# Kernel tuning notes

Measured on AMD Instinct MI355X. Metric: run time of the kernel, lower is better.

Reference implementation:

```python
import jax, jax.numpy as jnp
import numpy as np

# B groups, N packed tokens/group, D model dim, H heads, L layers, FF mlp hidden,
# M samples packed per group, C classes, PD patch_dim, NF/NT freq/time pos tables
B, N, D, H, L, FF, M, C, PD, NF, NT = 4, 1024, 768, 12, 12, 3072, 8, 527, 256, 8, 64


def _ln(x, g, b, eps=1e-6):
    m = jnp.mean(x, -1, keepdims=True)
    v = jnp.mean((x - m) ** 2, -1, keepdims=True)
    return (x - m) * jax.lax.rsqrt(v + eps) * g + b


def _attn(xq, xkv, Wq, bq, Wkv, bkv, Wo, bo, allowed):
    # allowed: [b, i, j] bool; faithful to source: NO 1/sqrt(d_head) scaling.
    b, i, _ = xq.shape
    j = xkv.shape[1]
    q = (xq @ Wq + bq).reshape(b, i, H, -1).transpose(0, 2, 1, 3)
    k, v = jnp.split(xkv @ Wkv + bkv, 2, axis=-1)
    k = k.reshape(b, j, H, -1).transpose(0, 2, 1, 3)
    v = v.reshape(b, j, H, -1).transpose(0, 2, 1, 3)
    dots = jnp.einsum('bhid,bhjd->bhij', q, k)
    neg = -jnp.finfo(dots.dtype).max
    dots = jnp.where(allowed[:, None, :, :], dots, neg)
    a = jax.nn.softmax(dots, axis=-1)
    out = jnp.einsum('bhij,bhjd->bhid', a, v).transpose(0, 2, 1, 3).reshape(b, i, -1)
    return out @ Wo + bo


def setup_inputs() -> dict:
    ks = iter(jax.random.split(jax.random.key(0), 48))
    rn = lambda shape, s=0.02: jax.random.normal(next(ks), shape, jnp.float32) * s
    return {
        'patches': jax.random.normal(next(ks), (B, N, PD), jnp.float32),
        'sample_ids': jnp.sort(jax.random.randint(next(ks), (B, N), 0, M), axis=-1).astype(jnp.int32),
        'key_pad': jnp.ones((B, N), bool),
        'freq_idx': jax.random.randint(next(ks), (B, N), 0, NF).astype(jnp.int32),
        'time_idx': jax.random.randint(next(ks), (B, N), 0, NT).astype(jnp.int32),
        'patch_W': rn((PD, D)), 'patch_b': jnp.zeros((D,)),
        'pos_f': rn((NF, D), 1.0), 'pos_t': rn((NT, D), 1.0),
        'ln1_g': jnp.ones((L, D)), 'ln1_b': jnp.zeros((L, D)),
        'Wq': rn((L, D, D)), 'bq': jnp.zeros((L, D)),
        'Wkv': rn((L, D, 2 * D)), 'bkv': jnp.zeros((L, 2 * D)),
        'Wo': rn((L, D, D)), 'bo': jnp.zeros((L, D)),
        'ln2_g': jnp.ones((L, D)), 'ln2_b': jnp.zeros((L, D)),
        'W1': rn((L, D, FF)), 'b1': jnp.zeros((L, FF)),
        'W2': rn((L, FF, D)), 'b2': jnp.zeros((L, D)),
        'norm_g': jnp.ones((D,)), 'norm_b': jnp.zeros((D,)),
        'pool_q': rn((D,), 1.0),
        'pool_Wq': rn((D, D)), 'pool_bq': jnp.zeros((D,)),
        'pool_Wkv': rn((D, 2 * D)), 'pool_bkv': jnp.zeros((2 * D,)),
        'pool_Wo': rn((D, D)), 'pool_bo': jnp.zeros((D,)),
        'mln_g': jnp.ones((D,)), 'mln_b': jnp.zeros((D,)),
        'head_W': rn((D, C)), 'head_b': jnp.zeros((C,)),
    }


def reference(patches, sample_ids, key_pad, freq_idx, time_idx, patch_W, patch_b, pos_f, pos_t,
              ln1_g, ln1_b, Wq, bq, Wkv, bkv, Wo, bo, ln2_g, ln2_b, W1, b1, W2, b2,
              norm_g, norm_b, pool_q, pool_Wq, pool_bq, pool_Wkv, pool_bkv, pool_Wo, pool_bo,
              mln_g, mln_b, head_W, head_b):
    # patch embed + factorized freq/time positional embedding
    x = patches @ patch_W + patch_b + pos_f[freq_idx] + pos_t[time_idx]  # [B, N, D]
    # block-diagonal attention within each packed sample + key-padding mask
    same = sample_ids[:, :, None] == sample_ids[:, None, :]
    allowed = same & key_pad[:, None, :]
    for l in range(L):
        h = _ln(x, ln1_g[l], ln1_b[l])
        x = x + _attn(h, h, Wq[l], bq[l], Wkv[l], bkv[l], Wo[l], bo[l], allowed)
        h = _ln(x, ln2_g[l], ln2_b[l])
        x = x + (jax.nn.gelu(h @ W1[l] + b1[l], approximate=False) @ W2[l] + b2[l])
    x = _ln(x, norm_g, norm_b)
    # attention pooling: one learned query per packed sample, attends only its own tokens
    queries = jnp.broadcast_to(pool_q, (B, M, D))
    pool_allowed = (sample_ids[:, None, :] == jnp.arange(M)[None, :, None]) & key_pad[:, None, :]
    pooled = _attn(queries, x, pool_Wq, pool_bq, pool_Wkv, pool_bkv, pool_Wo, pool_bo, pool_allowed)
    return _ln(pooled, mln_g, mln_b) @ head_W + head_b  # [B, M, C]
```

## Files before the change

### kernel.cpp

```cpp
#include <hip/hip_runtime.h>
#include <hip/hip_bf16.h>
#include <math.h>

#define BB   4
#define NN   1024
#define DD   768
#define HHH  12
#define LLL  12
#define FFD  3072
#define MMM  8
#define CCC  527
#define PDIM 256

typedef unsigned short u16;
typedef __attribute__((ext_vector_type(8))) short bf16x8;
typedef __attribute__((ext_vector_type(4))) float f32x4;

__device__ inline float b2f(u16 x) {
    union { float f; unsigned u; } c; c.u = ((unsigned)x) << 16; return c.f;
}
__device__ inline u16 f2b(float f) {
    __hip_bfloat16 h = __float2bfloat16(f);
    return *reinterpret_cast<u16*>(&h);
}

__device__ __forceinline__ void gl_lds16(const u16* g, const u16* l) {
    __builtin_amdgcn_global_load_lds(
        (const __attribute__((address_space(1))) unsigned int*)(unsigned long long)g,
        (__attribute__((address_space(3))) unsigned int*)(unsigned)(unsigned long long)l,
        16, 0, 0);
}

__global__ void k_pad_norm(const void* __restrict__ p, unsigned char* __restrict__ out, int n) {
    __shared__ int isInt;
    const int t = threadIdx.x;
    if (t == 0) isInt = 1;
    __syncthreads();
    const unsigned* up = (const unsigned*)p;
    for (int i = t; i < n / 4; i += 1024) {
        unsigned v = up[i];
        if (v > 1u) isInt = 0;
    }
    __syncthreads();
    const int* ip = (const int*)p;
    const unsigned char* cp = (const unsigned char*)p;
    const int mode = isInt;
    for (int i = t; i < n; i += 1024)
        out[i] = mode ? (unsigned char)(ip[i] != 0) : (unsigned char)(cp[i] != 0);
}

__global__ __launch_bounds__(256) void k_transpose_cvt(
    const float* __restrict__ src, u16* __restrict__ dst,
    int K, int N, long srcLS, long dstLS)
{
    __shared__ float t[32][33];
    const float* s = src + (size_t)blockIdx.z * srcLS;
    u16* d = dst + (size_t)blockIdx.z * dstLS;
    int n0 = blockIdx.x * 32, k0 = blockIdx.y * 32;
    int tx = threadIdx.x & 31, ty = threadIdx.x >> 5;
    #pragma unroll
    for (int i = 0; i < 32; i += 8)
        t[ty + i][tx] = s[(size_t)(k0 + ty + i) * N + n0 + tx];
    __syncthreads();
    #pragma unroll
    for (int i = 0; i < 32; i += 8)
        d[(size_t)(n0 + ty + i) * K + k0 + tx] = f2b(t[tx][ty + i]);
}

__global__ __launch_bounds__(256) void k_cvt(const float* __restrict__ s, u16* __restrict__ d, int n4) {
    int i = blockIdx.x * 256 + threadIdx.x;
    if (i >= n4) return;
    float4 v = ((const float4*)s)[i];
    union { u16 h[4]; uint2 u; } o;
    o.h[0] = f2b(v.x); o.h[1] = f2b(v.y); o.h[2] = f2b(v.z); o.h[3] = f2b(v.w);
    ((uint2*)d)[i] = o.u;
}

__global__ __launch_bounds__(256) void k_bias_pack(const float* __restrict__ bq,
                                                   const float* __restrict__ bkv,
                                                   float* __restrict__ bqkv) {
    int i = blockIdx.x * 256 + threadIdx.x;
    if (i >= LLL * 2304) return;
    int l = i / 2304, c = i % 2304;
    bqkv[i] = (c < 768) ? bq[l * 768 + c] : bkv[l * 1536 + (c - 768)];
}

__global__ void k_ranges(const int* __restrict__ sid, int2* __restrict__ qr, int2* __restrict__ pr) {
    int b = blockIdx.x, t = threadIdx.x;
    const int* s = sid + b * NN;
    if (t < 16) {
        int lo_id = s[t * 64], hi_id = s[t * 64 + 63];
        int lo = 0, hi = NN;
        while (lo < hi) { int mid = (lo + hi) >> 1; if (s[mid] < lo_id) lo = mid + 1; else hi = mid; }
        int l2 = 0, h2 = NN;
        while (l2 < h2) { int mid = (l2 + h2) >> 1; if (s[mid] <= hi_id) l2 = mid + 1; else h2 = mid; }
        qr[b * 16 + t] = make_int2(lo, l2);
    }
    if (t < MMM) {
        int l2 = 0, h2 = NN;
        while (l2 < h2) { int mid = (l2 + h2) >> 1; if (s[mid] < t) l2 = mid + 1; else h2 = mid; }
        int l3 = 0, h3 = NN;
        while (l3 < h3) { int mid = (l3 + h3) >> 1; if (s[mid] <= t) l3 = mid + 1; else h3 = mid; }
        pr[b * MMM + t] = make_int2(l2, l3);
    }
}

__device__ inline void stv(u16* p, float v) { *p = f2b(v); }
__device__ inline void stv(float* p, float v) { *p = v; }

template <typename OT>
__global__ __launch_bounds__(256) void k_ln(const float* __restrict__ x,
                                            const float* __restrict__ g,
                                            const float* __restrict__ b,
                                            OT* __restrict__ out) {
    int row = blockIdx.x;
    const float* xr = x + (size_t)row * DD;
    int t = threadIdx.x;
    float v[3], s1 = 0.f, s2 = 0.f;
    #pragma unroll
    for (int i = 0; i < 3; i++) { v[i] = xr[t + i * 256]; s1 += v[i]; s2 += v[i] * v[i]; }
    #pragma unroll
    for (int o = 32; o; o >>= 1) { s1 += __shfl_xor(s1, o); s2 += __shfl_xor(s2, o); }
    __shared__ float a1[4], a2[4];
    int w = t >> 6;
    if ((t & 63) == 0) { a1[w] = s1; a2[w] = s2; }
    __syncthreads();
    s1 = a1[0] + a1[1] + a1[2] + a1[3];
    s2 = a2[0] + a2[1] + a2[2] + a2[3];
    float mean = s1 * (1.f / DD);
    float var = s2 * (1.f / DD) - mean * mean;
    float rstd = rsqrtf(fmaxf(var, 0.f) + 1e-6f);
    #pragma unroll
    for (int i = 0; i < 3; i++) {
        int c = t + i * 256;
        stv(&out[(size_t)row * DD + c], (v[i] - mean) * rstd * g[c] + b[c]);
    }
}

template <int EPI, int BM>
__global__ __launch_bounds__(256) void k_gemm(
    const u16* __restrict__ A, int lda,
    const u16* __restrict__ Bt, int ldb,
    const float* __restrict__ bias,
    float* __restrict__ Cf, u16* __restrict__ Cb,
    const float* __restrict__ resid,
    int ldc, int K)
{
    constexpr int NR  = (BM == 128) ? 4 : 2;
    constexpr int ASZ = BM * 32;
    constexpr int BSZ = 128 * 32;
    __shared__ __align__(16) u16 As[3][ASZ];
    __shared__ __align__(16) u16 Bs[3][BSZ];
    const int row0 = blockIdx.y * BM, col0 = blockIdx.x * 128;
    const int t = threadIdx.x;
    const int w = t >> 6, lane = t & 63;
    const int wr = (BM == 128) ? (w >> 1) * 64 : 0;
    const int wc = (BM == 128) ? (w & 1) * 64 : w * 32;
    const int fr = lane & 15, fg = lane >> 4;
    const int srow = t >> 2, sseg = (t & 3) * 8;
    const u16* Ap = A + (size_t)(row0 + srow) * lda + sseg;
    const u16* Bp = Bt + (size_t)(col0 + srow) * ldb + sseg;
    const size_t lstep = (size_t)64 * lda, bstep = (size_t)64 * ldb;

    auto stage = [&](int buf, int k0) {
        #pragma unroll
        for (int i = 0; i < BM / 64; i++)
            gl_lds16(Ap + i * lstep + k0, &As[buf][i * 2048 + t * 8]);
        #pragma unroll
        for (int i = 0; i < 2; i++)
            gl_lds16(Bp + i * bstep + k0, &Bs[buf][i * 2048 + t * 8]);
    };

    f32x4 acc[4][NR];
    #pragma unroll
    for (int m = 0; m < 4; m++)
        #pragma unroll
        for (int n = 0; n < NR; n++) acc[m][n] = (f32x4){0.f, 0.f, 0.f, 0.f};

    const int nt = K >> 5;
    stage(0, 0);
    stage(1, 32);

    for (int kt = 0; kt < nt; ++kt) {
        if (kt + 1 < nt) {
            if constexpr (BM == 128) asm volatile("s_waitcnt vmcnt(4)" ::: "memory");
            else                     asm volatile("s_waitcnt vmcnt(3)" ::: "memory");
        } else {
            asm volatile("s_waitcnt vmcnt(0)" ::: "memory");
        }
        __builtin_amdgcn_s_barrier();
        __builtin_amdgcn_sched_barrier(0);
        if (kt + 2 < nt) stage((kt + 2) % 3, (kt + 2) * 32);
        const int cur = kt % 3;
        bf16x8 af[4], bfr[NR];
        #pragma unroll
        for (int m = 0; m < 4; m++) af[m] = *(const bf16x8*)&As[cur][(wr + m * 16 + fr) * 32 + fg * 8];
        #pragma unroll
        for (int n = 0; n < NR; n++) bfr[n] = *(const bf16x8*)&Bs[cur][(wc + n * 16 + fr) * 32 + fg * 8];
        #pragma unroll
        for (int m = 0; m < 4; m++)
            #pragma unroll
            for (int n = 0; n < NR; n++)
                acc[m][n] = __builtin_amdgcn_mfma_f32_16x16x32_bf16(af[m], bfr[n], acc[m][n], 0, 0, 0);
    }
    #pragma unroll
    for (int m = 0; m < 4; m++) {
        #pragma unroll
        for (int n = 0; n < NR; n++) {
            const int col = col0 + wc + n * 16 + fr;
            const float bb = bias[col];
            #pragma unroll
            for (int r = 0; r < 4; r++) {
                const size_t row = row0 + wr + m * 16 + fg * 4 + r;
                float v = acc[m][n][r] + bb;
                if (EPI == 0) {
                    Cb[row * ldc + col] = f2b(v);
                } else if (EPI == 1) {
                    Cf[row * ldc + col] = v + resid[row * ldc + col];
                } else if (EPI == 2) {
                    float gl = 0.5f * v * (1.f + erff(v * 0.70710678118f));
                    Cb[row * ldc + col] = f2b(gl);
                } else {
                    Cf[row * ldc + col] = v;
                }
            }
        }
    }
}

__global__ __launch_bounds__(256) void k_attn(
    const u16* __restrict__ qkv,
    const int* __restrict__ sid, const unsigned char* __restrict__ pad,
    const int2* __restrict__ qr,
    u16* __restrict__ outb)
{
    __shared__ __align__(16) u16 Qs[64][72];
    __shared__ __align__(16) u16 Ks[64][72];
    __shared__ __align__(16) u16 Vt[64][72];
    __shared__ __align__(16) u16 Ps[4][16][72];
    __shared__ int sidq[64];
    __shared__ int sidj[64];
    __shared__ int padj[64];
    const int b = blockIdx.z, h = blockIdx.y, qt = blockIdx.x;
    const int i0 = qt * 64;
    const int t = threadIdx.x, w = t >> 6, lane = t & 63;
    const int fr = lane & 15, fg = lane >> 4;
    const int srow = t >> 2, sseg = (t & 3) * 16;
    const size_t tokbase = (size_t)b * NN;
    const u16* qbase = qkv + (tokbase + i0) * 2304 + h * 64;
    *(uint4*)&Qs[srow][sseg]     = *(const uint4*)(qbase + (size_t)srow * 2304 + sseg);
    *(uint4*)&Qs[srow][sseg + 8] = *(const uint4*)(qbase + (size_t)srow * 2304 + sseg + 8);
    if (t < 64) sidq[t] = sid[tokbase + i0 + t];
    __syncthreads();
    bf16x8 qf0 = *(const bf16x8*)&Qs[w * 16 + fr][fg * 8];
    bf16x8 qf1 = *(const bf16x8*)&Qs[w * 16 + fr][32 + fg * 8];
    const int myrow = w * 16 + fg * 4;
    float m_run[4], l_run[4];
    f32x4 oacc[4];
    #pragma unroll
    for (int r = 0; r < 4; r++) { m_run[r] = -1e30f; l_run[r] = 0.f; }
    #pragma unroll
    for (int n = 0; n < 4; n++) oacc[n] = (f32x4){0.f, 0.f, 0.f, 0.f};
    const int2 rg = qr[b * 16 + qt];
    const u16* kbase = qkv + tokbase * 2304 + 768 + h * 64;
    const u16* vbase = qkv + tokbase * 2304 + 1536 + h * 64;

    for (int j0 = rg.x & ~63; j0 < rg.y; j0 += 64) {
        __syncthreads();
        *(uint4*)&Ks[srow][sseg]     = *(const uint4*)(kbase + (size_t)(j0 + srow) * 2304 + sseg);
        *(uint4*)&Ks[srow][sseg + 8] = *(const uint4*)(kbase + (size_t)(j0 + srow) * 2304 + sseg + 8);
        {
            uint4 v0 = *(const uint4*)(vbase + (size_t)(j0 + srow) * 2304 + sseg);
            uint4 v1 = *(const uint4*)(vbase + (size_t)(j0 + srow) * 2304 + sseg + 8);
            u16 tmp[16];
            *(uint4*)&tmp[0] = v0;
            *(uint4*)&tmp[8] = v1;
            #pragma unroll
            for (int e = 0; e < 16; e++) Vt[sseg + e][srow] = tmp[e];
        }
        if (t < 64) {
            sidj[t] = sid[tokbase + j0 + t];
            padj[t] = pad[tokbase + j0 + t];
        }
        __syncthreads();
        f32x4 s[4];
        #pragma unroll
        for (int nj = 0; nj < 4; nj++) {
            bf16x8 kf0 = *(const bf16x8*)&Ks[nj * 16 + fr][fg * 8];
            bf16x8 kf1 = *(const bf16x8*)&Ks[nj * 16 + fr][32 + fg * 8];
            f32x4 a = (f32x4){0.f, 0.f, 0.f, 0.f};
            a = __builtin_amdgcn_mfma_f32_16x16x32_bf16(qf0, kf0, a, 0, 0, 0);
            a = __builtin_amdgcn_mfma_f32_16x16x32_bf16(qf1, kf1, a, 0, 0, 0);
            s[nj] = a;
        }
        #pragma unroll
        for (int nj = 0; nj < 4; nj++) {
            const int jj = nj * 16 + fr;
            const int sj = sidj[jj];
            const int pd = padj[jj];
            #pragma unroll
            for (int r = 0; r < 4; r++) {
                const bool ok = pd && (sj == sidq[myrow + r]);
                s[nj][r] = ok ? s[nj][r] : -3e38f;
            }
        }
        float mnew[4], scale[4];
        #pragma unroll
        for (int r = 0; r < 4; r++) {
            float mx = fmaxf(fmaxf(s[0][r], s[1][r]), fmaxf(s[2][r], s[3][r]));
            #pragma unroll
            for (int o = 1; o < 16; o <<= 1) mx = fmaxf(mx, __shfl_xor(mx, o));
            mnew[r] = fmaxf(m_run[r], mx);
            scale[r] = __expf(m_run[r] - mnew[r]);
            m_run[r] = mnew[r];
        }
        #pragma unroll
        for (int r = 0; r < 4; r++) {
            float rs = 0.f;
            #pragma unroll
            for (int nj = 0; nj < 4; nj++) {
                float pv = __expf(s[nj][r] - mnew[r]);
                rs += pv;
                Ps[w][fg * 4 + r][nj * 16 + fr] = f2b(pv);
            }
            #pragma unroll
            for (int o = 1; o < 16; o <<= 1) rs += __shfl_xor(rs, o);
            l_run[r] = l_run[r] * scale[r] + rs;
        }
        #pragma unroll
        for (int n = 0; n < 4; n++)
            #pragma unroll
            for (int r = 0; r < 4; r++) oacc[n][r] *= scale[r];
        bf16x8 pa0 = *(const bf16x8*)&Ps[w][fr][fg * 8];
        bf16x8 pa1 = *(const bf16x8*)&Ps[w][fr][32 + fg * 8];
        #pragma unroll
        for (int nd = 0; nd < 4; nd++) {
            bf16x8 vf0 = *(const bf16x8*)&Vt[nd * 16 + fr][fg * 8];
            bf16x8 vf1 = *(const bf16x8*)&Vt[nd * 16 + fr][32 + fg * 8];
            oacc[nd] = __builtin_amdgcn_mfma_f32_16x16x32_bf16(pa0, vf0, oacc[nd], 0, 0, 0);
            oacc[nd] = __builtin_amdgcn_mfma_f32_16x16x32_bf16(pa1, vf1, oacc[nd], 0, 0, 0);
        }
    }
    float inv[4];
    #pragma unroll
    for (int r = 0; r < 4; r++) inv[r] = 1.f / l_run[r];
    #pragma unroll
    for (int nd = 0; nd < 4; nd++)
        #pragma unroll
        for (int r = 0; r < 4; r++)
            outb[(tokbase + i0 + myrow + r) * DD + h * 64 + nd * 16 + fr] = f2b(oacc[nd][r] * inv[r]);
}

__global__ __launch_bounds__(256) void k_posadd(float* __restrict__ x,
                                                const int* __restrict__ fidx, const int* __restrict__ tidx,
                                                const float* __restrict__ pf, const float* __restrict__ pt) {
    int row = blockIdx.x;
    int fi = fidx[row], ti = tidx[row];
    for (int c = threadIdx.x; c < DD; c += 256)
        x[(size_t)row * DD + c] += pf[(size_t)fi * DD + c] + pt[(size_t)ti * DD + c];
}

__global__ __launch_bounds__(64) void k_qvec(const float* __restrict__ pq, const float* __restrict__ Wq,
                                             const float* __restrict__ bq, float* __restrict__ qv) {
    int c = blockIdx.x;
    int l = threadIdx.x;
    float s = 0.f;
    #pragma unroll
    for (int d = l; d < DD; d += 64) s += pq[d] * Wq[(size_t)d * DD + c];
    #pragma unroll
    for (int o = 32; o; o >>= 1) s += __shfl_xor(s, o);
    if (l == 0) qv[c] = s + bq[c];
}

__global__ __launch_bounds__(256) void k_pool_attn(
    const float* __restrict__ qv, const u16* __restrict__ kv,
    const unsigned char* __restrict__ pad, const int2* __restrict__ pr,
    float* __restrict__ outp)
{
    const int idx = blockIdx.x;
    const int h = idx % HHH, bm = idx / HHH;
    const int b = bm >> 3, m = bm & 7;
    const int2 rg = pr[b * MMM + m];
    const int lo = rg.x, cnt = rg.y - rg.x;
    __shared__ float sc[NN];
    __shared__ float qsh[64];
    __shared__ float rbuf[4];
    __shared__ float vacc[4][64];
    if (threadIdx.x < 64) qsh[threadIdx.x] = qv[h * 64 + threadIdx.x];
    __syncthreads();
    for (int j = threadIdx.x; j < cnt; j += 256) {
        const u16* krow = kv + (size_t)(b * NN + lo + j) * 1536 + h * 64;
        float s = 0.f;
        #pragma unroll
        for (int dv = 0; dv < 8; dv++) {
            bf16x8 k8 = *(const bf16x8*)(krow + dv * 8);
            #pragma unroll
            for (int e = 0; e < 8; e++) s += qsh[dv * 8 + e] * b2f((u16)k8[e]);
        }
        sc[j] = pad[b * NN + lo + j] ? s : -3e38f;
    }
    __syncthreads();
    float mx = -3e38f;
    for (int j = threadIdx.x; j < cnt; j += 256) mx = fmaxf(mx, sc[j]);
    #pragma unroll
    for (int o = 32; o; o >>= 1) mx = fmaxf(mx, __shfl_xor(mx, o));
    if ((threadIdx.x & 63) == 0) rbuf[threadIdx.x >> 6] = mx;
    __syncthreads();
    mx = fmaxf(fmaxf(rbuf[0], rbuf[1]), fmaxf(rbuf[2], rbuf[3]));
    __syncthreads();
    float sm = 0.f;
    for (int j = threadIdx.x; j < cnt; j += 256) { float p = __expf(sc[j] - mx); sc[j] = p; sm += p; }
    #pragma unroll
    for (int o = 32; o; o >>= 1) sm += __shfl_xor(sm, o);
    if ((threadIdx.x & 63) == 0) rbuf[threadIdx.x >> 6] = sm;
    __syncthreads();
    sm = rbuf[0] + rbuf[1] + rbuf[2] + rbuf[3];
    const float inv = 1.f / sm;
    {
        const int d = threadIdx.x & 63, g = threadIdx.x >> 6;
        float acc = 0.f;
        for (int j = g; j < cnt; j += 4)
            acc += sc[j] * b2f(kv[(size_t)(b * NN + lo + j) * 1536 + 768 + h * 64 + d]);
        vacc[g][d] = acc;
        __syncthreads();
        if (g == 0)
            outp[(size_t)(b * MMM + m) * DD + h * 64 + d] =
                (vacc[0][d] + vacc[1][d] + vacc[2][d] + vacc[3][d]) * inv;
    }
}

__global__ __launch_bounds__(256) void k_small_mm(const float* __restrict__ A, const float* __restrict__ W,
                                                  const float* __restrict__ bias, float* __restrict__ out,
                                                  int N, int Kd) {
    const int row = blockIdx.y;
    const int cl = threadIdx.x & 63, kg = threadIdx.x >> 6;
    const int c = blockIdx.x * 64 + cl;
    const int cload = (c < N) ? c : (N - 1);
    __shared__ float As[DD];
    __shared__ float red[4][64];
    for (int d = threadIdx.x; d < Kd; d += 256) As[d] = A[(size_t)row * Kd + d];
    __syncthreads();
    const int kper = Kd >> 2;
    const int kbase = kg * kper;
    float s = 0.f;
    const float* w = W + (size_t)kbase * N + cload;
    #pragma unroll 4
    for (int i = 0; i < kper; i++) s += As[kbase + i] * w[(size_t)i * N];
    red[kg][cl] = s;
    __syncthreads();
    if (kg == 0 && c < N)
        out[(size_t)row * N + c] = red[0][cl] + red[1][cl] + red[2][cl] + red[3][cl] + bias[c];
}

extern "C" void kernel_launch(void* const* d_in, const int* in_sizes, int n_in,
                              void* d_out, int out_size, void* d_ws, size_t ws_size,
                              hipStream_t stream) {
    const float* patches   = (const float*)d_in[0];
    const int*   sample_ids= (const int*)d_in[1];
    const void*  key_pad_raw = (const void*)d_in[2];
    const int*   freq_idx  = (const int*)d_in[3];
    const int*   time_idx  = (const int*)d_in[4];
    const float* patch_W   = (const float*)d_in[5];
    const float* patch_b   = (const float*)d_in[6];
    const float* pos_f     = (const float*)d_in[7];
    const float* pos_t     = (const float*)d_in[8];
    const float* ln1_g     = (const float*)d_in[9];
    const float* ln1_b     = (const float*)d_in[10];
    const float* Wq        = (const float*)d_in[11];
    const float* bq        = (const float*)d_in[12];
    const float* Wkv       = (const float*)d_in[13];
    const float* bkv       = (const float*)d_in[14];
    const float* Wo        = (const float*)d_in[15];
    const float* bo        = (const float*)d_in[16];
    const float* ln2_g     = (const float*)d_in[17];
    const float* ln2_b     = (const float*)d_in[18];
    const float* W1        = (const float*)d_in[19];
    const float* b1        = (const float*)d_in[20];
    const float* W2        = (const float*)d_in[21];
    const float* b2        = (const float*)d_in[22];
    const float* norm_g    = (const float*)d_in[23];
    const float* norm_b    = (const float*)d_in[24];
    const float* pool_q    = (const float*)d_in[25];
    const float* pool_Wq   = (const float*)d_in[26];
    const float* pool_bq   = (const float*)d_in[27];
    const float* pool_Wkv  = (const float*)d_in[28];
    const float* pool_bkv  = (const float*)d_in[29];
    const float* pool_Wo   = (const float*)d_in[30];
    const float* pool_bo   = (const float*)d_in[31];
    const float* mln_g     = (const float*)d_in[32];
    const float* mln_b     = (const float*)d_in[33];
    const float* head_W    = (const float*)d_in[34];
    const float* head_b    = (const float*)d_in[35];
    float* outp = (float*)d_out;
    (void)in_sizes; (void)n_in; (void)out_size; (void)ws_size;

    char* ws = (char*)d_ws;
    size_t off = 0;
    auto alloc = [&](size_t bytes) -> void* {
        void* p = (void*)(ws + off);
        off += (bytes + 255) & ~(size_t)255;
        return p;
    };
    u16* WqkvT    = (u16*)alloc((size_t)LLL * 2304 * 768 * 2);
    u16* WoT      = (u16*)alloc((size_t)LLL * 768 * 768 * 2);
    u16* W1T      = (u16*)alloc((size_t)LLL * 3072 * 768 * 2);
    u16* W2T      = (u16*)alloc((size_t)LLL * 768 * 3072 * 2);
    u16* patchWT  = (u16*)alloc((size_t)768 * 256 * 2);
    u16* poolWkvT = (u16*)alloc((size_t)1536 * 768 * 2);
    float* bqkv   = (float*)alloc((size_t)LLL * 2304 * 4);
    unsigned char* pad_u8 = (unsigned char*)alloc(BB * NN);
    float* x      = (float*)alloc((size_t)4096 * 768 * 4);
    u16* hbuf     = (u16*)alloc((size_t)4096 * 768 * 2);
    u16* qkvb     = (u16*)alloc((size_t)4096 * 2304 * 2);
    u16* attno    = (u16*)alloc((size_t)4096 * 768 * 2);
    u16* mid      = (u16*)alloc((size_t)4096 * 3072 * 2);
    u16* patch_bf = mid;
    u16* xn       = attno;
    u16* poolkv   = qkvb;
    float* qvec   = (float*)alloc(768 * 4);
    float* pooled_pre = (float*)alloc(32 * 768 * 4);
    float* pooled2    = (float*)alloc(32 * 768 * 4);
    float* mlnout     = (float*)alloc(32 * 768 * 4);
    int2* qr = (int2*)alloc(4 * 16 * sizeof(int2));
    int2* pr = (int2*)alloc(4 * 8 * sizeof(int2));

    k_pad_norm<<<1, 1024, 0, stream>>>(key_pad_raw, pad_u8, BB * NN);
    k_transpose_cvt<<<dim3(24, 24, LLL), 256, 0, stream>>>(Wq, WqkvT, 768, 768, (long)768 * 768, (long)2304 * 768);
    k_transpose_cvt<<<dim3(48, 24, LLL), 256, 0, stream>>>(Wkv, WqkvT + (size_t)768 * 768, 768, 1536, (long)768 * 1536, (long)2304 * 768);
    k_transpose_cvt<<<dim3(24, 24, LLL), 256, 0, stream>>>(Wo, WoT, 768, 768, (long)768 * 768, (long)768 * 768);
    k_transpose_cvt<<<dim3(96, 24, LLL), 256, 0, stream>>>(W1, W1T, 768, 3072, (long)768 * 3072, (long)3072 * 768);
    k_transpose_cvt<<<dim3(24, 96, LLL), 256, 0, stream>>>(W2, W2T, 3072, 768, (long)3072 * 768, (long)768 * 3072);
    k_transpose_cvt<<<dim3(24, 8, 1), 256, 0, stream>>>(patch_W, patchWT, 256, 768, 0, 0);
    k_transpose_cvt<<<dim3(48, 24, 1), 256, 0, stream>>>(pool_Wkv, poolWkvT, 768, 1536, 0, 0);
    k_cvt<<<1024, 256, 0, stream>>>(patches, patch_bf, 4096 * 256 / 4);
    k_bias_pack<<<(LLL * 2304 + 255) / 256, 256, 0, stream>>>(bq, bkv, bqkv);
    k_ranges<<<4, 64, 0, stream>>>(sample_ids, qr, pr);

    k_gemm<3, 64><<<dim3(6, 64), 256, 0, stream>>>(patch_bf, 256, patchWT, 256, patch_b, x, nullptr, nullptr, 768, 256);
    k_posadd<<<4096, 256, 0, stream>>>(x, freq_idx, time_idx, pos_f, pos_t);

    for (int l = 0; l < LLL; l++) {
        k_ln<u16><<<4096, 256, 0, stream>>>(x, ln1_g + l * 768, ln1_b + l * 768, hbuf);
        k_gemm<0, 128><<<dim3(18, 32), 256, 0, stream>>>(hbuf, 768, WqkvT + (size_t)l * 2304 * 768, 768,
                                                         bqkv + l * 2304, nullptr, qkvb, nullptr, 2304, 768);
        k_attn<<<dim3(16, 12, 4), 256, 0, stream>>>(qkvb, sample_ids, pad_u8, qr, attno);
        k_gemm<1, 64><<<dim3(6, 64), 256, 0, stream>>>(attno, 768, WoT + (size_t)l * 768 * 768, 768,
                                                       bo + l * 768, x, nullptr, x, 768, 768);
        k_ln<u16><<<4096, 256, 0, stream>>>(x, ln2_g + l * 768, ln2_b + l * 768, hbuf);
        k_gemm<2, 128><<<dim3(24, 32), 256, 0, stream>>>(hbuf, 768, W1T + (size_t)l * 3072 * 768, 768,
                                                         b1 + l * 3072, nullptr, mid, nullptr, 3072, 768);
        k_gemm<1, 64><<<dim3(6, 64), 256, 0, stream>>>(mid, 3072, W2T + (size_t)l * 768 * 3072, 3072,
                                                       b2 + l * 768, x, nullptr, x, 768, 3072);
    }

    k_ln<u16><<<4096, 256, 0, stream>>>(x, norm_g, norm_b, xn);
    k_gemm<0, 128><<<dim3(12, 32), 256, 0, stream>>>(xn, 768, poolWkvT, 768, pool_bkv, nullptr, poolkv, nullptr, 1536, 768);
    k_qvec<<<768, 64, 0, stream>>>(pool_q, pool_Wq, pool_bq, qvec);
    k_pool_attn<<<BB * MMM * HHH, 256, 0, stream>>>(qvec, poolkv, pad_u8, pr, pooled_pre);
    k_small_mm<<<dim3(12, 32), 256, 0, stream>>>(pooled_pre, pool_Wo, pool_bo, pooled2, 768, 768);
    k_ln<float><<<32, 256, 0, stream>>>(pooled2, mln_g, mln_b, mlnout);
    k_small_mm<<<dim3(9, 32), 256, 0, stream>>>(mlnout, head_W, head_b, outp, 527, 768);
}
```

Measured before the change: 2.178 ms.

## Swizzle GEMM blocks across XCDs, prefetch attention K/V, skew V layout

The GEMM kernel remaps its linear block id so that, when the grid size is a multiple of 8, each XCD gets a contiguous range of output tiles. The aim is better L2 reuse of the A and B panels. The attention kernel now loads the next K/V tile, sample ids and pad flags into registers while the current tile is being computed, overlapping global loads with MFMA work. The transposed V buffer in LDS gets a per-16-row skew to cut bank conflicts on the scattered transpose writes. The costs are extra registers for the prefetch and some more index arithmetic.

```diff
diff --git a/kernel.cpp b/kernel.cpp
--- a/kernel.cpp
+++ b/kernel.cpp
@@ -151,7 +151,11 @@
     constexpr int BSZ = 128 * 32;
     __shared__ __align__(16) u16 As[3][ASZ];
     __shared__ __align__(16) u16 Bs[3][BSZ];
-    const int row0 = blockIdx.y * BM, col0 = blockIdx.x * 128;
+    const int gx = gridDim.x;
+    const int nwg = gx * gridDim.y;
+    int bid = blockIdx.y * gx + blockIdx.x;
+    if ((nwg & 7) == 0) bid = (bid & 7) * (nwg >> 3) + (bid >> 3);
+    const int row0 = (bid / gx) * BM, col0 = (bid % gx) * 128;
     const int t = threadIdx.x;
     const int w = t >> 6, lane = t & 63;
     const int wr = (BM == 128) ? (w >> 1) * 64 : 0;
@@ -236,7 +240,7 @@
 {
     __shared__ __align__(16) u16 Qs[64][72];
     __shared__ __align__(16) u16 Ks[64][72];
-    __shared__ __align__(16) u16 Vt[64][72];
+    __shared__ __align__(16) u16 VtL[64 * 72 + 32];
     __shared__ __align__(16) u16 Ps[4][16][72];
     __shared__ int sidq[64];
     __shared__ int sidj[64];
@@ -265,24 +269,41 @@
     const u16* kbase = qkv + tokbase * 2304 + 768 + h * 64;
     const u16* vbase = qkv + tokbase * 2304 + 1536 + h * 64;
 
-    for (int j0 = rg.x & ~63; j0 < rg.y; j0 += 64) {
+    uint4 rk0, rk1, rv0, rv1;
+    int rsid = 0, rpad = 0;
+    const int jstart = rg.x & ~63;
+    {
+        const size_t ro = (size_t)(jstart + srow) * 2304;
+        rk0 = *(const uint4*)(kbase + ro + sseg);
+        rk1 = *(const uint4*)(kbase + ro + sseg + 8);
+        rv0 = *(const uint4*)(vbase + ro + sseg);
+        rv1 = *(const uint4*)(vbase + ro + sseg + 8);
+        if (t < 64) { rsid = sid[tokbase + jstart + t]; rpad = pad[tokbase + jstart + t]; }
+    }
+
+    for (int j0 = jstart; j0 < rg.y; j0 += 64) {
         __syncthreads();
-        *(uint4*)&Ks[srow][sseg]     = *(const uint4*)(kbase + (size_t)(j0 + srow) * 2304 + sseg);
-        *(uint4*)&Ks[srow][sseg + 8] = *(const uint4*)(kbase + (size_t)(j0 + srow) * 2304 + sseg + 8);
+        *(uint4*)&Ks[srow][sseg]     = rk0;
+        *(uint4*)&Ks[srow][sseg + 8] = rk1;
         {
-            uint4 v0 = *(const uint4*)(vbase + (size_t)(j0 + srow) * 2304 + sseg);
-            uint4 v1 = *(const uint4*)(vbase + (size_t)(j0 + srow) * 2304 + sseg + 8);
             u16 tmp[16];
-            *(uint4*)&tmp[0] = v0;
-            *(uint4*)&tmp[8] = v1;
-            #pragma unroll
-            for (int e = 0; e < 16; e++) Vt[sseg + e][srow] = tmp[e];
-        }
-        if (t < 64) {
-            sidj[t] = sid[tokbase + j0 + t];
-            padj[t] = pad[tokbase + j0 + t];
-        }
+            *(uint4*)&tmp[0] = rv0;
+            *(uint4*)&tmp[8] = rv1;
+            const int goff = (sseg >> 4) << 3;
+            #pragma unroll
+            for (int e = 0; e < 16; e++)
+                VtL[(sseg + e) * 72 + goff + srow] = tmp[e];
+        }
+        if (t < 64) { sidj[t] = rsid; padj[t] = rpad; }
         __syncthreads();
+        if (j0 + 64 < rg.y) {
+            const size_t ro = (size_t)(j0 + 64 + srow) * 2304;
+            rk0 = *(const uint4*)(kbase + ro + sseg);
+            rk1 = *(const uint4*)(kbase + ro + sseg + 8);
+            rv0 = *(const uint4*)(vbase + ro + sseg);
+            rv1 = *(const uint4*)(vbase + ro + sseg + 8);
+            if (t < 64) { rsid = sid[tokbase + j0 + 64 + t]; rpad = pad[tokbase + j0 + 64 + t]; }
+        }
         f32x4 s[4];
         #pragma unroll
         for (int nj = 0; nj < 4; nj++) {
@@ -335,8 +356,8 @@
         bf16x8 pa1 = *(const bf16x8*)&Ps[w][fr][32 + fg * 8];
         #pragma unroll
         for (int nd = 0; nd < 4; nd++) {
-            bf16x8 vf0 = *(const bf16x8*)&Vt[nd * 16 + fr][fg * 8];
-            bf16x8 vf1 = *(const bf16x8*)&Vt[nd * 16 + fr][32 + fg * 8];
+            bf16x8 vf0 = *(const bf16x8*)&VtL[(nd * 16 + fr) * 72 + nd * 8 + fg * 8];
+            bf16x8 vf1 = *(const bf16x8*)&VtL[(nd * 16 + fr) * 72 + nd * 8 + 32 + fg * 8];
             oacc[nd] = __builtin_amdgcn_mfma_f32_16x16x32_bf16(pa0, vf0, oacc[nd], 0, 0, 0);
             oacc[nd] = __builtin_amdgcn_mfma_f32_16x16x32_bf16(pa1, vf1, oacc[nd], 0, 0, 0);
         }
```

After: 2.060 ms. 1.06x faster.
